# Performance work log

Measured on AMD Instinct MI355X. Metric: run time of the kernel, lower is better.

The kernel has to match this reference:

```python
import jax, jax.numpy as jnp
import numpy as np
from jax import lax

EPS = 1e-5
K = 32
S1, S2 = 512, 256


def bn_relu(x, gamma, beta, axes):
    # BatchNorm in training mode (batch statistics, biased variance) + ReLU.
    mean = jnp.mean(x, axis=axes, keepdims=True)
    var = jnp.var(x, axis=axes, keepdims=True)
    return jax.nn.relu((x - mean) * lax.rsqrt(var + EPS) * gamma + beta)


def fps(xyz, s):
    # Farthest point sampling, deterministic start at index 0. xyz: [N,3] -> [s] indices
    N = xyz.shape[0]
    def body(carry, _):
        dist, far = carry
        d = jnp.sum((xyz - xyz[far]) ** 2, axis=-1)
        dist = jnp.minimum(dist, d)
        return (dist, jnp.argmax(dist).astype(jnp.int32)), far
    init = (jnp.full((N,), 1e10, xyz.dtype), jnp.int32(0))
    _, idx = lax.scan(body, init, None, length=s)
    return idx


def sample_and_knn_group(s, k, coords, features):
    # coords: [B,N,3], features: [B,N,D]
    fps_idx = jax.vmap(lambda c: fps(c, s))(coords)                      # [B,s]
    new_xyz = jnp.take_along_axis(coords, fps_idx[..., None], axis=1)   # [B,s,3]
    new_feat = jnp.take_along_axis(features, fps_idx[..., None], axis=1)  # [B,s,D]
    # squared euclidean distances [B,s,N]
    d2 = (jnp.sum(new_xyz ** 2, -1)[..., None]
          - 2.0 * jnp.einsum('bsc,bnc->bsn', new_xyz, coords)
          + jnp.sum(coords ** 2, -1)[:, None, :])
    _, knn_idx = lax.top_k(-d2, k)                                       # [B,s,k]
    grouped = jax.vmap(lambda f, i: f[i])(features, knn_idx)             # [B,s,k,D]
    rel = grouped - new_feat[:, :, None, :]
    agg = jnp.concatenate([rel, jnp.broadcast_to(new_feat[:, :, None, :], rel.shape)], axis=-1)  # [B,s,k,2D]
    return new_xyz, agg


def sg_block(s, coords, feats, w1, cb1, g1, b1, w2, cb2, g2, b2):
    new_xyz, agg = sample_and_knn_group(s, K, coords, feats)
    h = bn_relu(jnp.einsum('bskc,oc->bsko', agg, w1) + cb1, g1, b1, (0, 1, 2))
    h = bn_relu(jnp.einsum('bskc,oc->bsko', h, w2) + cb2, g2, b2, (0, 1, 2))
    return new_xyz, jnp.max(h, axis=2)  # max over k neighbors -> [B,s,O]


def setup_inputs() -> dict:
    key = jax.random.key(0)
    ks = jax.random.split(key, 8)
    B, N = 16, 2048
    sc = 0.05
    return {
        'x': jax.random.normal(ks[0], (B, 3, N), jnp.float32),
        'emb_w1': jax.random.normal(ks[1], (64, 3), jnp.float32) * sc,
        'emb_g1': jnp.ones((64,), jnp.float32), 'emb_b1': jnp.zeros((64,), jnp.float32),
        'emb_w2': jax.random.normal(ks[2], (64, 64), jnp.float32) * sc,
        'emb_g2': jnp.ones((64,), jnp.float32), 'emb_b2': jnp.zeros((64,), jnp.float32),
        'sg1_w1': jax.random.normal(ks[3], (128, 128), jnp.float32) * sc,
        'sg1_cb1': jnp.zeros((128,), jnp.float32),
        'sg1_g1': jnp.ones((128,), jnp.float32), 'sg1_b1': jnp.zeros((128,), jnp.float32),
        'sg1_w2': jax.random.normal(ks[4], (128, 128), jnp.float32) * sc,
        'sg1_cb2': jnp.zeros((128,), jnp.float32),
        'sg1_g2': jnp.ones((128,), jnp.float32), 'sg1_b2': jnp.zeros((128,), jnp.float32),
        'sg2_w1': jax.random.normal(ks[5], (512, 256), jnp.float32) * sc,
        'sg2_cb1': jnp.zeros((512,), jnp.float32),
        'sg2_g1': jnp.ones((512,), jnp.float32), 'sg2_b1': jnp.zeros((512,), jnp.float32),
        'sg2_w2': jax.random.normal(ks[6], (512, 512), jnp.float32) * sc,
        'sg2_cb2': jnp.zeros((512,), jnp.float32),
        'sg2_g2': jnp.ones((512,), jnp.float32), 'sg2_b2': jnp.zeros((512,), jnp.float32),
    }


def reference(x, emb_w1, emb_g1, emb_b1, emb_w2, emb_g2, emb_b2,
              sg1_w1, sg1_cb1, sg1_g1, sg1_b1, sg1_w2, sg1_cb2, sg1_g2, sg1_b2,
              sg2_w1, sg2_cb1, sg2_g1, sg2_b1, sg2_w2, sg2_cb2, sg2_g2, sg2_b2):
    xyz = jnp.transpose(x, (0, 2, 1))  # [B,N,3]
    f = bn_relu(jnp.einsum('bnc,oc->bno', xyz, emb_w1), emb_g1, emb_b1, (0, 1))   # [B,N,64]
    f = bn_relu(jnp.einsum('bnc,oc->bno', f, emb_w2), emb_g2, emb_b2, (0, 1))
    xyz1, f1 = sg_block(S1, xyz, f, sg1_w1, sg1_cb1, sg1_g1, sg1_b1,
                        sg1_w2, sg1_cb2, sg1_g2, sg1_b2)   # [B,512,128]
    _, f2 = sg_block(S2, xyz1, f1, sg2_w1, sg2_cb1, sg2_g1, sg2_b1,
                     sg2_w2, sg2_cb2, sg2_g2, sg2_b2)      # [B,256,512]
    return jnp.transpose(f2, (0, 2, 1))  # [B,512,256] to match torch [B,C,s]
```

## Files before the change

### kernel.cpp

```cpp
#include <hip/hip_runtime.h>
#include <hip/hip_bf16.h>

#define EPS_BN 1e-5f
constexpr int BB = 16, NN = 2048, SS1 = 512, SS2 = 256, KNb = 32;

typedef short bf16x8 __attribute__((ext_vector_type(8)));
typedef float f32x4 __attribute__((ext_vector_type(4)));

__device__ inline float bflo(unsigned u) { return __uint_as_float(u << 16); }
__device__ inline float bfhi(unsigned u) { return __uint_as_float(u & 0xffff0000u); }
__device__ inline unsigned short f2bf_bits(float v) {
  __hip_bfloat16 h = __float2bfloat16(v);
  return *reinterpret_cast<unsigned short*>(&h);
}
__device__ inline unsigned fmono(float v) {
  int b = __float_as_int(v);
  return (unsigned)(b ^ ((b >> 31) | 0x80000000));
}

template <int CTRL>
__device__ inline void dpp_step_min(unsigned& hi, unsigned& lo) {
  unsigned hs = (unsigned)__builtin_amdgcn_update_dpp((int)hi, (int)hi, CTRL, 0xF, 0xF, false);
  unsigned ls = (unsigned)__builtin_amdgcn_update_dpp((int)lo, (int)lo, CTRL, 0xF, 0xF, false);
  bool take = (hs < hi) || (hs == hi && ls < lo);
  hi = take ? hs : hi; lo = take ? ls : lo;
}
template <int CTRL>
__device__ inline void dpp_step_maxv_minidx(unsigned& hi, unsigned& lo) {
  unsigned hs = (unsigned)__builtin_amdgcn_update_dpp((int)hi, (int)hi, CTRL, 0xF, 0xF, false);
  unsigned ls = (unsigned)__builtin_amdgcn_update_dpp((int)lo, (int)lo, CTRL, 0xF, 0xF, false);
  bool take = (hs > hi) || (hs == hi && ls < lo);
  hi = take ? hs : hi; lo = take ? ls : lo;
}
__device__ inline void dpp_chain_min(unsigned& hi, unsigned& lo) {
  dpp_step_min<0x111>(hi, lo); dpp_step_min<0x112>(hi, lo);
  dpp_step_min<0x114>(hi, lo); dpp_step_min<0x118>(hi, lo);
  dpp_step_min<0x142>(hi, lo); dpp_step_min<0x143>(hi, lo);
}
__device__ inline void dpp_chain_maxv_minidx(unsigned& hi, unsigned& lo) {
  dpp_step_maxv_minidx<0x111>(hi, lo); dpp_step_maxv_minidx<0x112>(hi, lo);
  dpp_step_maxv_minidx<0x114>(hi, lo); dpp_step_maxv_minidx<0x118>(hi, lo);
  dpp_step_maxv_minidx<0x142>(hi, lo); dpp_step_maxv_minidx<0x143>(hi, lo);
}
__device__ inline int dpp_reduce_min_idx(unsigned hi, unsigned lo) {
  dpp_chain_min(hi, lo);
  return __builtin_amdgcn_readlane((int)lo, 63);
}

__global__ void k_transpose(const float* __restrict__ x, float* __restrict__ xyz) {
  int idx = blockIdx.x * blockDim.x + threadIdx.x;
  if (idx >= BB * NN * 3) return;
  int c = idx % 3; int n = (idx / 3) % NN; int b = idx / (3 * NN);
  xyz[idx] = x[((size_t)b * 3 + c) * NN + n];
}

__global__ void k_emb1(const float* __restrict__ xyz, const float* __restrict__ w,
                       float* __restrict__ out) {
  int idx = blockIdx.x * blockDim.x + threadIdx.x;
  if (idx >= BB * NN * 64) return;
  int o = idx & 63; int pt = idx >> 6;
  const float* p = xyz + (size_t)pt * 3;
  const float* wr = w + o * 3;
  out[idx] = p[0] * wr[0] + p[1] * wr[1] + p[2] * wr[2];
}

__global__ void k_emb2(const float* __restrict__ fin, const float* __restrict__ w,
                       float* __restrict__ out) {
  int idx = blockIdx.x * blockDim.x + threadIdx.x;
  if (idx >= BB * NN * 64) return;
  int o = idx & 63; int pt = idx >> 6;
  const float* f = fin + (size_t)pt * 64;
  const float* wr = w + o * 64;
  float acc = 0.f;
#pragma unroll
  for (int c = 0; c < 64; c++) acc += f[c] * wr[c];
  out[idx] = acc;
}

__global__ __launch_bounds__(256) void k_stats_co(const float* __restrict__ d,
                                                  double* __restrict__ rsum,
                                                  double* __restrict__ rsq) {
  __shared__ float ls[64], lq[64];
  int t = threadIdx.x;
  if (t < 64) { ls[t] = 0.f; lq[t] = 0.f; }
  __syncthreads();
  size_t base = (size_t)blockIdx.x * 8192 + t * 4;
  float a0 = 0, a1 = 0, a2 = 0, a3 = 0, q0 = 0, q1 = 0, q2 = 0, q3 = 0;
  for (int it = 0; it < 8; it++) {
    float4 v = *(const float4*)(d + base + (size_t)it * 1024);
    a0 += v.x; q0 += v.x * v.x;
    a1 += v.y; q1 += v.y * v.y;
    a2 += v.z; q2 += v.z * v.z;
    a3 += v.w; q3 += v.w * v.w;
  }
  int c0 = (t * 4) & 63;
  atomicAdd(&ls[c0], a0); atomicAdd(&lq[c0], q0);
  atomicAdd(&ls[c0 + 1], a1); atomicAdd(&lq[c0 + 1], q1);
  atomicAdd(&ls[c0 + 2], a2); atomicAdd(&lq[c0 + 2], q2);
  atomicAdd(&ls[c0 + 3], a3); atomicAdd(&lq[c0 + 3], q3);
  __syncthreads();
  if (t < 64) {
    int rep = blockIdx.x & 63;
    atomicAdd(&rsum[(size_t)rep * 64 + t], (double)ls[t]);
    atomicAdd(&rsq[(size_t)rep * 64 + t], (double)lq[t]);
  }
}

__global__ void k_normrelu(float* __restrict__ data, const float* __restrict__ scale,
                           const float* __restrict__ shift, int total, int O) {
  int idx = blockIdx.x * blockDim.x + threadIdx.x;
  if (idx >= total) return;
  int o = idx % O;
  data[idx] = fmaxf(data[idx] * scale[o] + shift[o], 0.f);
}

template <int N>
__global__ __launch_bounds__(256, 1) void k_fps_mw(const float* __restrict__ xyz, int S,
                                                   int* __restrict__ fpsidx,
                                                   float* __restrict__ newxyz) {
  constexpr int PPL = N / 256;
  int b = blockIdx.x; int t = threadIdx.x;
  int w = t >> 6;
  __shared__ float sx[N], sy[N], sz[N];
  __shared__ unsigned combH[2][4], combL[2][4];
  float px[PPL], py[PPL], pz[PPL], ds[PPL];
#pragma unroll
  for (int r = 0; r < PPL; r++) {
    int i = r * 256 + t;
    size_t base = ((size_t)b * N + i) * 3;
    float xx = xyz[base], yy = xyz[base + 1], zz = xyz[base + 2];
    px[r] = xx; py[r] = yy; pz[r] = zz;
    float ox = xx, oy = yy, oz = zz;
    asm volatile("" : "+v"(ox), "+v"(oy), "+v"(oz));
    sx[i] = ox; sy[i] = oy; sz[i] = oz;
    ds[r] = 1e10f;
  }
  __syncthreads();
  int far = 0; int p = 0;
  for (int it = 0; it < S; it++) {
    float fx = sx[far], fy = sy[far], fz = sz[far];
    if (t == 0) {
      fpsidx[b * S + it] = far;
      size_t ob = ((size_t)b * S + it) * 3;
      newxyz[ob] = fx; newxyz[ob + 1] = fy; newxyz[ob + 2] = fz;
    }
    float mv0 = -1.f, mv1 = -1.f, mv2 = -1.f, mv3 = -1.f;
    int mi0 = 0, mi1 = 0, mi2 = 0, mi3 = 0;
#pragma unroll
    for (int r = 0; r < PPL; r++) {
      float dx = px[r] - fx, dy = py[r] - fy, dz = pz[r] - fz;
      float d = dx * dx + dy * dy + dz * dz;
      float nd = d < ds[r] ? d : ds[r];
      ds[r] = nd;
      int gi = r * 256 + t;
      if ((r & 3) == 0) { bool tk = nd > mv0; mv0 = tk ? nd : mv0; mi0 = tk ? gi : mi0; }
      else if ((r & 3) == 1) { bool tk = nd > mv1; mv1 = tk ? nd : mv1; mi1 = tk ? gi : mi1; }
      else if ((r & 3) == 2) { bool tk = nd > mv2; mv2 = tk ? nd : mv2; mi2 = tk ? gi : mi2; }
      else { bool tk = nd > mv3; mv3 = tk ? nd : mv3; mi3 = tk ? gi : mi3; }
    }
    { bool tk = (mv1 > mv0) || (mv1 == mv0 && mi1 < mi0);
      mv0 = tk ? mv1 : mv0; mi0 = tk ? mi1 : mi0; }
    { bool tk = (mv3 > mv2) || (mv3 == mv2 && mi3 < mi2);
      mv2 = tk ? mv3 : mv2; mi2 = tk ? mi3 : mi2; }
    { bool tk = (mv2 > mv0) || (mv2 == mv0 && mi2 < mi0);
      mv0 = tk ? mv2 : mv0; mi0 = tk ? mi2 : mi0; }
    unsigned hi = __float_as_uint(mv0);
    unsigned lo = (unsigned)mi0;
    dpp_chain_maxv_minidx(hi, lo);
    unsigned rh = (unsigned)__builtin_amdgcn_readlane((int)hi, 63);
    unsigned rl = (unsigned)__builtin_amdgcn_readlane((int)lo, 63);
    combH[p][w] = rh;
    combL[p][w] = rl;
    __syncthreads();
    unsigned bh = combH[p][0], bl = combL[p][0];
#pragma unroll
    for (int ww = 1; ww < 4; ww++) {
      unsigned oh = combH[p][ww], ol = combL[p][ww];
      bool take = (oh > bh) || (oh == bh && ol < bl);
      bh = take ? oh : bh; bl = take ? ol : bl;
    }
    far = (int)bl;
    p ^= 1;
  }
}

template <int N, int S>
__global__ __launch_bounds__(64, 1) void k_knn_wave(const float* __restrict__ pts,
                                                    const float* __restrict__ ctr,
                                                    int* __restrict__ knn) {
  constexpr int PPL = N / 64;
  int blk = blockIdx.x; int lane = threadIdx.x;
  int b = blk / S;
  float cx = ctr[(size_t)blk * 3], cy = ctr[(size_t)blk * 3 + 1], cz = ctr[(size_t)blk * 3 + 2];
  float cn = cx * cx + cy * cy + cz * cz;
  float d2[PPL];
#pragma unroll
  for (int r = 0; r < PPL; r++) {
    int i = r * 64 + lane;
    size_t pb = ((size_t)b * N + i) * 3;
    float xx = pts[pb], yy = pts[pb + 1], zz = pts[pb + 2];
    d2[r] = cn - 2.f * (cx * xx + cy * yy + cz * zz) + (xx * xx + yy * yy + zz * zz);
  }
  for (int kk = 0; kk < KNb; kk++) {
    float a0 = d2[0], a1 = d2[1], a2 = d2[2], a3 = d2[3];
#pragma unroll
    for (int r = 4; r < PPL; r += 4) {
      a0 = fminf(a0, d2[r]); a1 = fminf(a1, d2[r + 1]);
      a2 = fminf(a2, d2[r + 2]); a3 = fminf(a3, d2[r + 3]);
    }
    float m = fminf(fminf(a0, a1), fminf(a2, a3));
    int cand[PPL];
#pragma unroll
    for (int r = 0; r < PPL; r++) cand[r] = (d2[r] == m) ? (r * 64 + lane) : 0x7fffffff;
#pragma unroll
    for (int st = PPL / 2; st > 0; st >>= 1)
#pragma unroll
      for (int r = 0; r < st; r++) cand[r] = cand[r] < cand[r + st] ? cand[r] : cand[r + st];
    int widx = dpp_reduce_min_idx(fmono(m), (unsigned)cand[0]);
    if (lane == 0) knn[(size_t)blk * KNb + kk] = widx;
    int wr = widx >> 6, wl = widx & 63;
#pragma unroll
    for (int r = 0; r < PPL; r++) d2[r] = (r == wr && lane == wl) ? 3.4e38f : d2[r];
  }
}

__global__ void k_f2bf(const float* __restrict__ w, __hip_bfloat16* __restrict__ o, int n) {
  int i = blockIdx.x * blockDim.x + threadIdx.x;
  if (i < n) o[i] = __float2bfloat16(w[i]);
}

template <int D>
__global__ __launch_bounds__(256) void k_gather(const float* __restrict__ feat, int N,
                                                const int* __restrict__ fpsidx,
                                                const int* __restrict__ knn, int S,
                                                __hip_bfloat16* __restrict__ A) {
  int blk = blockIdx.x; int b = blk / S; int t = threadIdx.x;
  __shared__ float cf[D]; __shared__ int nbr[KNb];
  if (t < KNb) nbr[t] = knn[(size_t)blk * KNb + t];
  int center = fpsidx[blk];
  for (int c = t; c < D; c += 256) cf[c] = feat[((size_t)b * N + center) * D + c];
  __syncthreads();
  for (int i = t; i < KNb * D; i += 256) {
    int kk = i / D, c = i - kk * D;
    float v = feat[((size_t)b * N + nbr[kk]) * D + c];
    size_t row = (size_t)blk * KNb + kk;
    A[row * (2 * D) + c] = __float2bfloat16(v - cf[c]);
    A[row * (2 * D) + D + c] = __float2bfloat16(cf[c]);
  }
}

template <int K, int EPI>
__global__ __launch_bounds__(256) void k_mgemm(
    const __hip_bfloat16* __restrict__ A, const __hip_bfloat16* __restrict__ W,
    int N, int Mtiles, const float* __restrict__ bias,
    __hip_bfloat16* __restrict__ Hout,
    float* __restrict__ maxb, float* __restrict__ minb,
    double* __restrict__ rsum, double* __restrict__ rsq) {
  constexpr int SP = 40;
  int bm = blockIdx.x % Mtiles; int bn = blockIdx.x / Mtiles;
  int t = threadIdx.x; int w = t >> 6; int lane = t & 63;
  int wm = w & 1, wn = w >> 1; int quad = lane >> 4; int l15 = lane & 15;
  __shared__ short As[128 * SP];
  __shared__ short Ws[128 * SP];
  f32x4 acc[4][4];
  f32x4 zero = {0.f, 0.f, 0.f, 0.f};
#pragma unroll
  for (int i = 0; i < 4; i++)
#pragma unroll
    for (int j = 0; j < 4; j++) acc[i][j] = zero;

  int srow = t >> 2, sseg = t & 3;
  const short* Ag = (const short*)A;
  const short* Wg = (const short*)W;
  size_t arow0 = (size_t)bm * 128;
  size_t wrow0 = (size_t)bn * 128;

  for (int k0 = 0; k0 < K; k0 += 32) {
    __syncthreads();
    uint4 a0 = *(const uint4*)(Ag + (arow0 + srow) * K + k0 + sseg * 8);
    uint4 a1 = *(const uint4*)(Ag + (arow0 + srow + 64) * K + k0 + sseg * 8);
    uint4 b0 = *(const uint4*)(Wg + (wrow0 + srow) * K + k0 + sseg * 8);
    uint4 b1 = *(const uint4*)(Wg + (wrow0 + srow + 64) * K + k0 + sseg * 8);
    *(uint4*)(As + srow * SP + sseg * 8) = a0;
    *(uint4*)(As + (srow + 64) * SP + sseg * 8) = a1;
    *(uint4*)(Ws + srow * SP + sseg * 8) = b0;
    *(uint4*)(Ws + (srow + 64) * SP + sseg * 8) = b1;
    __syncthreads();
    bf16x8 af[4], bfr[4];
#pragma unroll
    for (int i = 0; i < 4; i++)
      af[i] = *(const bf16x8*)(As + (wm * 64 + i * 16 + l15) * SP + quad * 8);
#pragma unroll
    for (int j = 0; j < 4; j++)
      bfr[j] = *(const bf16x8*)(Ws + (wn * 64 + j * 16 + l15) * SP + quad * 8);
#pragma unroll
    for (int i = 0; i < 4; i++)
#pragma unroll
      for (int j = 0; j < 4; j++)
        acc[i][j] = __builtin_amdgcn_mfma_f32_16x16x32_bf16(af[i], bfr[j], acc[i][j], 0, 0, 0);
  }

  if constexpr (EPI == 0) {
    int rep = blockIdx.x & 63;
#pragma unroll
    for (int j = 0; j < 4; j++) {
      int col = bn * 128 + wn * 64 + j * 16 + l15;
      float bs = bias[col];
      float su = 0.f, sq = 0.f;
#pragma unroll
      for (int i = 0; i < 4; i++)
#pragma unroll
        for (int r = 0; r < 4; r++) {
          int row = bm * 128 + wm * 64 + i * 16 + quad * 4 + r;
          float v = acc[i][j][r] + bs;
          Hout[(size_t)row * N + col] = __float2bfloat16(v);
          su += v; sq += v * v;
        }
      atomicAdd(&rsum[(size_t)rep * N + col], (double)su);
      atomicAdd(&rsq[(size_t)rep * N + col], (double)sq);
    }
  } else {
    __shared__ float buf[128][33];
    for (int s = 0; s < 4; s++) {
      __syncthreads();
      if (wn == (s >> 1)) {
        int jb = 2 * (s & 1);
#pragma unroll
        for (int jj = 0; jj < 2; jj++) {
          int j = jb + jj;
          int lcol = jj * 16 + l15;
          float bs = bias[bn * 128 + s * 32 + lcol];
#pragma unroll
          for (int i = 0; i < 4; i++)
#pragma unroll
            for (int r = 0; r < 4; r++)
              buf[wm * 64 + i * 16 + quad * 4 + r][lcol] = acc[i][j][r] + bs;
        }
      }
      __syncthreads();
      if (t < 128) {
        int g = t >> 5, c = t & 31;
        float mx = -3.4e38f, mn = 3.4e38f, su = 0.f, sq = 0.f;
#pragma unroll
        for (int r = 0; r < 32; r++) {
          float v = buf[g * 32 + r][c];
          mx = fmaxf(mx, v); mn = fminf(mn, v);
          su += v; sq += v * v;
        }
        int col = bn * 128 + s * 32 + c;
        size_t gidx = (size_t)bm * 4 + g;
        maxb[gidx * N + col] = mx;
        minb[gidx * N + col] = mn;
        int rep = blockIdx.x & 63;
        atomicAdd(&rsum[(size_t)rep * N + col], (double)su);
        atomicAdd(&rsq[(size_t)rep * N + col], (double)sq);
      }
    }
  }
}

__global__ __launch_bounds__(256) void k_bnrelu(__hip_bfloat16* __restrict__ Hm, int O, int iters,
                                                const float* __restrict__ sc,
                                                const float* __restrict__ sh) {
  int t = threadIdx.x;
  size_t base = (size_t)blockIdx.x * 2048 * iters + t * 8;
  int c0 = (t * 8) & (O - 1);
  float s[8], h[8];
#pragma unroll
  for (int j = 0; j < 8; j++) { s[j] = sc[c0 + j]; h[j] = sh[c0 + j]; }
  unsigned* Hu = (unsigned*)Hm;
  for (int it = 0; it < iters; it++) {
    size_t e = (base + (size_t)it * 2048) / 2;
    uint4 raw = *(uint4*)(Hu + e);
    unsigned ws_[4] = {raw.x, raw.y, raw.z, raw.w};
    unsigned out[4];
#pragma unroll
    for (int k = 0; k < 4; k++) {
      float v0 = fmaxf(bflo(ws_[k]) * s[2 * k] + h[2 * k], 0.f);
      float v1 = fmaxf(bfhi(ws_[k]) * s[2 * k + 1] + h[2 * k + 1], 0.f);
      out[k] = (unsigned)f2bf_bits(v0) | ((unsigned)f2bf_bits(v1) << 16);
    }
    uint4 o4 = {out[0], out[1], out[2], out[3]};
    *(uint4*)(Hu + e) = o4;
  }
}

__global__ void k_finalize(const double* __restrict__ rsum, const double* __restrict__ rsq,
                           int O, int rows,
                           const float* __restrict__ gamma, const float* __restrict__ beta,
                           float* __restrict__ scale, float* __restrict__ shift) {
  int o = blockIdx.x * blockDim.x + threadIdx.x;
  if (o >= O) return;
  double s = 0, s2 = 0;
  for (int r = 0; r < 64; r++) { s += rsum[(size_t)r * O + o]; s2 += rsq[(size_t)r * O + o]; }
  double mean = s / rows;
  double var = s2 / rows - mean * mean;
  float sc = gamma[o] * rsqrtf((float)var + EPS_BN);
  scale[o] = sc; shift[o] = beta[o] - (float)mean * sc;
}

__global__ void k_final_feat(const float* __restrict__ maxb, const float* __restrict__ minb,
                             const float* __restrict__ scale, const float* __restrict__ shift,
                             float* __restrict__ out, int total, int O) {
  int idx = blockIdx.x * blockDim.x + threadIdx.x;
  if (idx >= total) return;
  int o = idx % O; float sc = scale[o];
  float sel = sc > 0.f ? maxb[idx] : minb[idx];
  out[idx] = fmaxf(sel * sc + shift[o], 0.f);
}

__global__ void k_final_out(const float* __restrict__ maxb, const float* __restrict__ minb,
                            const float* __restrict__ scale, const float* __restrict__ shift,
                            float* __restrict__ out) {
  int idx = blockIdx.x * blockDim.x + threadIdx.x;
  if (idx >= BB * SS2 * 512) return;
  int o = idx % 512; int si = (idx / 512) % SS2; int b = idx / (512 * SS2);
  float sc = scale[o];
  float sel = sc > 0.f ? maxb[idx] : minb[idx];
  out[((size_t)b * 512 + o) * SS2 + si] = fmaxf(sel * sc + shift[o], 0.f);
}

extern "C" void kernel_launch(void* const* d_in, const int* in_sizes, int n_in,
                              void* d_out, int out_size, void* d_ws, size_t ws_size,
                              hipStream_t stream) {
  const float* x       = (const float*)d_in[0];
  const float* emb_w1  = (const float*)d_in[1];
  const float* emb_g1  = (const float*)d_in[2];
  const float* emb_b1  = (const float*)d_in[3];
  const float* emb_w2  = (const float*)d_in[4];
  const float* emb_g2  = (const float*)d_in[5];
  const float* emb_b2  = (const float*)d_in[6];
  const float* sg1_w1  = (const float*)d_in[7];
  const float* sg1_cb1 = (const float*)d_in[8];
  const float* sg1_g1  = (const float*)d_in[9];
  const float* sg1_b1  = (const float*)d_in[10];
  const float* sg1_w2  = (const float*)d_in[11];
  const float* sg1_cb2 = (const float*)d_in[12];
  const float* sg1_g2  = (const float*)d_in[13];
  const float* sg1_b2  = (const float*)d_in[14];
  const float* sg2_w1  = (const float*)d_in[15];
  const float* sg2_cb1 = (const float*)d_in[16];
  const float* sg2_g1  = (const float*)d_in[17];
  const float* sg2_b1  = (const float*)d_in[18];
  const float* sg2_w2  = (const float*)d_in[19];
  const float* sg2_cb2 = (const float*)d_in[20];
  const float* sg2_g2  = (const float*)d_in[21];
  const float* sg2_b2  = (const float*)d_in[22];

  char* ws = (char*)d_ws;
  size_t off = 0;
  auto alloc = [&](size_t bytes) -> size_t {
    size_t cur = off; off += (bytes + 255) & ~(size_t)255; return cur;
  };
  float* xyz  = (float*)(ws + alloc((size_t)BB * NN * 3 * 4));
  float* fA   = (float*)(ws + alloc((size_t)BB * NN * 64 * 4));
  float* fB   = (float*)(ws + alloc((size_t)BB * NN * 64 * 4));
  float* f1   = (float*)(ws + alloc((size_t)BB * SS1 * 128 * 4));
  float* nx1  = (float*)(ws + alloc((size_t)BB * SS1 * 3 * 4));
  float* nx2  = (float*)(ws + alloc((size_t)BB * SS2 * 3 * 4));
  int* fps1   = (int*)(ws + alloc((size_t)BB * SS1 * 4));
  int* fps2   = (int*)(ws + alloc((size_t)BB * SS2 * 4));
  int* knn1   = (int*)(ws + alloc((size_t)BB * SS1 * KNb * 4));
  int* knn2   = (int*)(ws + alloc((size_t)BB * SS2 * KNb * 4));
  float* maxb = (float*)(ws + alloc((size_t)BB * SS2 * 512 * 4));
  float* minb = (float*)(ws + alloc((size_t)BB * SS2 * 512 * 4));
  float* scbuf = (float*)(ws + alloc((size_t)12 * 512 * 4));
  float* sc11 = scbuf + 4 * 512, *sh11 = scbuf + 5 * 512;
  float* sc12 = scbuf + 6 * 512, *sh12 = scbuf + 7 * 512;
  float* sc21 = scbuf + 8 * 512, *sh21 = scbuf + 9 * 512;
  float* sc22 = scbuf + 10 * 512, *sh22 = scbuf + 11 * 512;
  float* sc_e1 = scbuf + 0 * 512, *sh_e1 = scbuf + 1 * 512;
  float* sc_e2 = scbuf + 2 * 512, *sh_e2 = scbuf + 3 * 512;
  size_t statsz = (size_t)12 * 64 * 512 * 8;
  char* statz = ws + alloc(statsz);
  double* st = (double*)statz;
  double* rsA = st + 0 * 64 * 512, *rqA = st + 1 * 64 * 512;
  double* rsB = st + 2 * 64 * 512, *rqB = st + 3 * 64 * 512;
  double* rsC = st + 4 * 64 * 512, *rqC = st + 5 * 64 * 512;
  double* rsD = st + 6 * 64 * 512, *rqD = st + 7 * 64 * 512;
  double* rsE1 = st + 8 * 64 * 512, *rqE1 = st + 9 * 64 * 512;
  double* rsE2 = st + 10 * 64 * 512, *rqE2 = st + 11 * 64 * 512;
  __hip_bfloat16* wb11 = (__hip_bfloat16*)(ws + alloc(128 * 128 * 2));
  __hip_bfloat16* wb12 = (__hip_bfloat16*)(ws + alloc(128 * 128 * 2));
  __hip_bfloat16* wb21 = (__hip_bfloat16*)(ws + alloc(512 * 256 * 2));
  __hip_bfloat16* wb22 = (__hip_bfloat16*)(ws + alloc(512 * 512 * 2));
  __hip_bfloat16* Abuf = (__hip_bfloat16*)(ws + alloc((size_t)262144 * 128 * 2));
  __hip_bfloat16* Hbuf = (__hip_bfloat16*)(ws + alloc((size_t)131072 * 512 * 2));

  hipMemsetAsync(statz, 0, statsz, stream);

  const int thr = 256;
  k_transpose<<<(BB * NN * 3 + thr - 1) / thr, thr, 0, stream>>>(x, xyz);
  k_emb1<<<(BB * NN * 64 + thr - 1) / thr, thr, 0, stream>>>(xyz, emb_w1, fA);
  k_stats_co<<<256, 256, 0, stream>>>(fA, rsE1, rqE1);
  k_finalize<<<1, 64, 0, stream>>>(rsE1, rqE1, 64, BB * NN, emb_g1, emb_b1, sc_e1, sh_e1);
  k_normrelu<<<(BB * NN * 64 + thr - 1) / thr, thr, 0, stream>>>(fA, sc_e1, sh_e1, BB * NN * 64, 64);
  k_emb2<<<(BB * NN * 64 + thr - 1) / thr, thr, 0, stream>>>(fA, emb_w2, fB);
  k_stats_co<<<256, 256, 0, stream>>>(fB, rsE2, rqE2);
  k_finalize<<<1, 64, 0, stream>>>(rsE2, rqE2, 64, BB * NN, emb_g2, emb_b2, sc_e2, sh_e2);
  k_normrelu<<<(BB * NN * 64 + thr - 1) / thr, thr, 0, stream>>>(fB, sc_e2, sh_e2, BB * NN * 64, 64);

  k_f2bf<<<(128 * 128 + 255) / 256, 256, 0, stream>>>(sg1_w1, wb11, 128 * 128);
  k_f2bf<<<(128 * 128 + 255) / 256, 256, 0, stream>>>(sg1_w2, wb12, 128 * 128);
  k_f2bf<<<(512 * 256 + 255) / 256, 256, 0, stream>>>(sg2_w1, wb21, 512 * 256);
  k_f2bf<<<(512 * 512 + 255) / 256, 256, 0, stream>>>(sg2_w2, wb22, 512 * 512);

  k_fps_mw<NN><<<BB, 256, 0, stream>>>(xyz, SS1, fps1, nx1);
  k_knn_wave<NN, SS1><<<BB * SS1, 64, 0, stream>>>(xyz, nx1, knn1);

  k_gather<64><<<BB * SS1, 256, 0, stream>>>(fB, NN, fps1, knn1, SS1, Abuf);
  k_mgemm<128, 0><<<2048, 256, 0, stream>>>(Abuf, wb11, 128, 2048, sg1_cb1, Hbuf,
                                            nullptr, nullptr, rsA, rqA);
  k_finalize<<<1, 128, 0, stream>>>(rsA, rqA, 128, 262144, sg1_g1, sg1_b1, sc11, sh11);
  k_bnrelu<<<1024, 256, 0, stream>>>(Hbuf, 128, 16, sc11, sh11);
  k_mgemm<128, 1><<<2048, 256, 0, stream>>>(Hbuf, wb12, 128, 2048, sg1_cb2, nullptr,
                                            maxb, minb, rsB, rqB);
  k_finalize<<<1, 128, 0, stream>>>(rsB, rqB, 128, 262144, sg1_g2, sg1_b2, sc12, sh12);
  k_final_feat<<<(BB * SS1 * 128 + thr - 1) / thr, thr, 0, stream>>>(maxb, minb, sc12, sh12,
                                                                     f1, BB * SS1 * 128, 128);

  k_fps_mw<SS1><<<BB, 256, 0, stream>>>(nx1, SS2, fps2, nx2);
  k_knn_wave<SS1, SS2><<<BB * SS2, 64, 0, stream>>>(nx1, nx2, knn2);

  k_gather<128><<<BB * SS2, 256, 0, stream>>>(f1, SS1, fps2, knn2, SS2, Abuf);
  k_mgemm<256, 0><<<1024 * 4, 256, 0, stream>>>(Abuf, wb21, 512, 1024, sg2_cb1, Hbuf,
                                                nullptr, nullptr, rsC, rqC);
  k_finalize<<<4, 128, 0, stream>>>(rsC, rqC, 512, 131072, sg2_g1, sg2_b1, sc21, sh21);
  k_bnrelu<<<2048, 256, 0, stream>>>(Hbuf, 512, 16, sc21, sh21);
  k_mgemm<512, 1><<<1024 * 4, 256, 0, stream>>>(Hbuf, wb22, 512, 1024, sg2_cb2, nullptr,
                                                maxb, minb, rsD, rqD);
  k_finalize<<<4, 128, 0, stream>>>(rsD, rqD, 512, 131072, sg2_g2, sg2_b2, sc22, sh22);
  k_final_out<<<(BB * SS2 * 512 + thr - 1) / thr, thr, 0, stream>>>(maxb, minb, sc22, sh22,
                                                                    (float*)d_out);
}
```

Baseline: 1.465 ms.

## Fuse BN+ReLU into next GEMM's A-load and streamline FPS argmax

Removes the standalone k_bnrelu passes and instead applies the batch-norm scale/shift and ReLU to A tiles as they are loaded in the second GEMM of each block, using per-channel scale/shift staged in shared memory. This drops a full read-modify-write of the hidden activation buffer. The second GEMM redoes the normalization once per N-tile (several times for the 512-wide layer), which adds ALU work in the load path. FPS also packs xyz into a float4 in shared memory and splits the argmax into a max-value pass followed by a min-index tree, to cut per-point select work in the serial loop.

New measurement: 1.339 ms. 1.09x faster.

```diff
diff --git a/kernel.cpp b/kernel.cpp
--- a/kernel.cpp
+++ b/kernel.cpp
@@ -16,6 +16,11 @@
 __device__ inline unsigned fmono(float v) {
   int b = __float_as_int(v);
   return (unsigned)(b ^ ((b >> 31) | 0x80000000));
+}
+__device__ inline unsigned bn2(unsigned u, float s0, float h0, float s1, float h1) {
+  float v0 = fmaxf(bflo(u) * s0 + h0, 0.f);
+  float v1 = fmaxf(bfhi(u) * s1 + h1, 0.f);
+  return (unsigned)f2bf_bits(v0) | ((unsigned)f2bf_bits(v1) << 16);
 }
 
 template <int CTRL>
@@ -121,7 +126,7 @@
   constexpr int PPL = N / 256;
   int b = blockIdx.x; int t = threadIdx.x;
   int w = t >> 6;
-  __shared__ float sx[N], sy[N], sz[N];
+  __shared__ float4 sxyz[N];
   __shared__ unsigned combH[2][4], combL[2][4];
   float px[PPL], py[PPL], pz[PPL], ds[PPL];
 #pragma unroll
@@ -132,40 +137,42 @@
     px[r] = xx; py[r] = yy; pz[r] = zz;
     float ox = xx, oy = yy, oz = zz;
     asm volatile("" : "+v"(ox), "+v"(oy), "+v"(oz));
-    sx[i] = ox; sy[i] = oy; sz[i] = oz;
+    float4 o4 = {ox, oy, oz, 0.f};
+    sxyz[i] = o4;
     ds[r] = 1e10f;
   }
   __syncthreads();
   int far = 0; int p = 0;
   for (int it = 0; it < S; it++) {
-    float fx = sx[far], fy = sy[far], fz = sz[far];
+    float4 f4 = sxyz[far];
+    float fx = f4.x, fy = f4.y, fz = f4.z;
     if (t == 0) {
       fpsidx[b * S + it] = far;
       size_t ob = ((size_t)b * S + it) * 3;
       newxyz[ob] = fx; newxyz[ob + 1] = fy; newxyz[ob + 2] = fz;
     }
-    float mv0 = -1.f, mv1 = -1.f, mv2 = -1.f, mv3 = -1.f;
-    int mi0 = 0, mi1 = 0, mi2 = 0, mi3 = 0;
+    float mm0 = -1.f, mm1 = -1.f, mm2 = -1.f, mm3 = -1.f;
 #pragma unroll
     for (int r = 0; r < PPL; r++) {
       float dx = px[r] - fx, dy = py[r] - fy, dz = pz[r] - fz;
       float d = dx * dx + dy * dy + dz * dz;
       float nd = d < ds[r] ? d : ds[r];
       ds[r] = nd;
-      int gi = r * 256 + t;
-      if ((r & 3) == 0) { bool tk = nd > mv0; mv0 = tk ? nd : mv0; mi0 = tk ? gi : mi0; }
-      else if ((r & 3) == 1) { bool tk = nd > mv1; mv1 = tk ? nd : mv1; mi1 = tk ? gi : mi1; }
-      else if ((r & 3) == 2) { bool tk = nd > mv2; mv2 = tk ? nd : mv2; mi2 = tk ? gi : mi2; }
-      else { bool tk = nd > mv3; mv3 = tk ? nd : mv3; mi3 = tk ? gi : mi3; }
-    }
-    { bool tk = (mv1 > mv0) || (mv1 == mv0 && mi1 < mi0);
-      mv0 = tk ? mv1 : mv0; mi0 = tk ? mi1 : mi0; }
-    { bool tk = (mv3 > mv2) || (mv3 == mv2 && mi3 < mi2);
-      mv2 = tk ? mv3 : mv2; mi2 = tk ? mi3 : mi2; }
-    { bool tk = (mv2 > mv0) || (mv2 == mv0 && mi2 < mi0);
-      mv0 = tk ? mv2 : mv0; mi0 = tk ? mi2 : mi0; }
-    unsigned hi = __float_as_uint(mv0);
-    unsigned lo = (unsigned)mi0;
+      if ((r & 3) == 0) mm0 = nd > mm0 ? nd : mm0;
+      else if ((r & 3) == 1) mm1 = nd > mm1 ? nd : mm1;
+      else if ((r & 3) == 2) mm2 = nd > mm2 ? nd : mm2;
+      else mm3 = nd > mm3 ? nd : mm3;
+    }
+    float m = fmaxf(fmaxf(mm0, mm1), fmaxf(mm2, mm3));
+    int cand[PPL];
+#pragma unroll
+    for (int r = 0; r < PPL; r++) cand[r] = (ds[r] == m) ? (r * 256 + t) : 0x7fffffff;
+#pragma unroll
+    for (int st = PPL / 2; st > 0; st >>= 1)
+#pragma unroll
+      for (int r = 0; r < st; r++) cand[r] = cand[r] < cand[r + st] ? cand[r] : cand[r + st];
+    unsigned hi = __float_as_uint(m);
+    unsigned lo = (unsigned)cand[0];
     dpp_chain_maxv_minidx(hi, lo);
     unsigned rh = (unsigned)__builtin_amdgcn_readlane((int)hi, 63);
     unsigned rl = (unsigned)__builtin_amdgcn_readlane((int)lo, 63);
@@ -249,10 +256,11 @@
   }
 }
 
-template <int K, int EPI>
+template <int K, int EPI, bool BNA>
 __global__ __launch_bounds__(256) void k_mgemm(
     const __hip_bfloat16* __restrict__ A, const __hip_bfloat16* __restrict__ W,
     int N, int Mtiles, const float* __restrict__ bias,
+    const float* __restrict__ bnsc, const float* __restrict__ bnsh,
     __hip_bfloat16* __restrict__ Hout,
     float* __restrict__ maxb, float* __restrict__ minb,
     double* __restrict__ rsum, double* __restrict__ rsq) {
@@ -262,6 +270,10 @@
   int wm = w & 1, wn = w >> 1; int quad = lane >> 4; int l15 = lane & 15;
   __shared__ short As[128 * SP];
   __shared__ short Ws[128 * SP];
+  __shared__ float scs[BNA ? K : 1], shs[BNA ? K : 1];
+  if constexpr (BNA) {
+    for (int i = t; i < K; i += 256) { scs[i] = bnsc[i]; shs[i] = bnsh[i]; }
+  }
   f32x4 acc[4][4];
   f32x4 zero = {0.f, 0.f, 0.f, 0.f};
 #pragma unroll
@@ -281,6 +293,20 @@
     uint4 a1 = *(const uint4*)(Ag + (arow0 + srow + 64) * K + k0 + sseg * 8);
     uint4 b0 = *(const uint4*)(Wg + (wrow0 + srow) * K + k0 + sseg * 8);
     uint4 b1 = *(const uint4*)(Wg + (wrow0 + srow + 64) * K + k0 + sseg * 8);
+    if constexpr (BNA) {
+      int cb = k0 + sseg * 8;
+      float s[8], h[8];
+#pragma unroll
+      for (int q = 0; q < 8; q++) { s[q] = scs[cb + q]; h[q] = shs[cb + q]; }
+      a0.x = bn2(a0.x, s[0], h[0], s[1], h[1]);
+      a0.y = bn2(a0.y, s[2], h[2], s[3], h[3]);
+      a0.z = bn2(a0.z, s[4], h[4], s[5], h[5]);
+      a0.w = bn2(a0.w, s[6], h[6], s[7], h[7]);
+      a1.x = bn2(a1.x, s[0], h[0], s[1], h[1]);
+      a1.y = bn2(a1.y, s[2], h[2], s[3], h[3]);
+      a1.z = bn2(a1.z, s[4], h[4], s[5], h[5]);
+      a1.w = bn2(a1.w, s[6], h[6], s[7], h[7]);
+    }
     *(uint4*)(As + srow * SP + sseg * 8) = a0;
     *(uint4*)(As + (srow + 64) * SP + sseg * 8) = a1;
     *(uint4*)(Ws + srow * SP + sseg * 8) = b0;
@@ -356,32 +382,6 @@
         atomicAdd(&rsq[(size_t)rep * N + col], (double)sq);
       }
     }
-  }
-}
-
-__global__ __launch_bounds__(256) void k_bnrelu(__hip_bfloat16* __restrict__ Hm, int O, int iters,
-                                                const float* __restrict__ sc,
-                                                const float* __restrict__ sh) {
-  int t = threadIdx.x;
-  size_t base = (size_t)blockIdx.x * 2048 * iters + t * 8;
-  int c0 = (t * 8) & (O - 1);
-  float s[8], h[8];
-#pragma unroll
-  for (int j = 0; j < 8; j++) { s[j] = sc[c0 + j]; h[j] = sh[c0 + j]; }
-  unsigned* Hu = (unsigned*)Hm;
-  for (int it = 0; it < iters; it++) {
-    size_t e = (base + (size_t)it * 2048) / 2;
-    uint4 raw = *(uint4*)(Hu + e);
-    unsigned ws_[4] = {raw.x, raw.y, raw.z, raw.w};
-    unsigned out[4];
-#pragma unroll
-    for (int k = 0; k < 4; k++) {
-      float v0 = fmaxf(bflo(ws_[k]) * s[2 * k] + h[2 * k], 0.f);
-      float v1 = fmaxf(bfhi(ws_[k]) * s[2 * k + 1] + h[2 * k + 1], 0.f);
-      out[k] = (unsigned)f2bf_bits(v0) | ((unsigned)f2bf_bits(v1) << 16);
-    }
-    uint4 o4 = {out[0], out[1], out[2], out[3]};
-    *(uint4*)(Hu + e) = o4;
   }
 }
 
@@ -509,12 +509,13 @@
   k_knn_wave<NN, SS1><<<BB * SS1, 64, 0, stream>>>(xyz, nx1, knn1);
 
   k_gather<64><<<BB * SS1, 256, 0, stream>>>(fB, NN, fps1, knn1, SS1, Abuf);
-  k_mgemm<128, 0><<<2048, 256, 0, stream>>>(Abuf, wb11, 128, 2048, sg1_cb1, Hbuf,
-                                            nullptr, nullptr, rsA, rqA);
+  k_mgemm<128, 0, false><<<2048, 256, 0, stream>>>(Abuf, wb11, 128, 2048, sg1_cb1,
+                                                   nullptr, nullptr, Hbuf,
+                                                   nullptr, nullptr, rsA, rqA);
   k_finalize<<<1, 128, 0, stream>>>(rsA, rqA, 128, 262144, sg1_g1, sg1_b1, sc11, sh11);
-  k_bnrelu<<<1024, 256, 0, stream>>>(Hbuf, 128, 16, sc11, sh11);
-  k_mgemm<128, 1><<<2048, 256, 0, stream>>>(Hbuf, wb12, 128, 2048, sg1_cb2, nullptr,
-                                            maxb, minb, rsB, rqB);
+  k_mgemm<128, 1, true><<<2048, 256, 0, stream>>>(Hbuf, wb12, 128, 2048, sg1_cb2,
+                                                  sc11, sh11, nullptr,
+                                                  maxb, minb, rsB, rqB);
   k_finalize<<<1, 128, 0, stream>>>(rsB, rqB, 128, 262144, sg1_g2, sg1_b2, sc12, sh12);
   k_final_feat<<<(BB * SS1 * 128 + thr - 1) / thr, thr, 0, stream>>>(maxb, minb, sc12, sh12,
                                                                      f1, BB * SS1 * 128, 128);
@@ -523,12 +524,13 @@
   k_knn_wave<SS1, SS2><<<BB * SS2, 64, 0, stream>>>(nx1, nx2, knn2);
 
   k_gather<128><<<BB * SS2, 256, 0, stream>>>(f1, SS1, fps2, knn2, SS2, Abuf);
-  k_mgemm<256, 0><<<1024 * 4, 256, 0, stream>>>(Abuf, wb21, 512, 1024, sg2_cb1, Hbuf,
-                                                nullptr, nullptr, rsC, rqC);
+  k_mgemm<256, 0, false><<<1024 * 4, 256, 0, stream>>>(Abuf, wb21, 512, 1024, sg2_cb1,
+                                                       nullptr, nullptr, Hbuf,
+                                                       nullptr, nullptr, rsC, rqC);
   k_finalize<<<4, 128, 0, stream>>>(rsC, rqC, 512, 131072, sg2_g1, sg2_b1, sc21, sh21);
-  k_bnrelu<<<2048, 256, 0, stream>>>(Hbuf, 512, 16, sc21, sh21);
-  k_mgemm<512, 1><<<1024 * 4, 256, 0, stream>>>(Hbuf, wb22, 512, 1024, sg2_cb2, nullptr,
-                                                maxb, minb, rsD, rqD);
+  k_mgemm<512, 1, true><<<1024 * 4, 256, 0, stream>>>(Hbuf, wb22, 512, 1024, sg2_cb2,
+                                                      sc21, sh21, nullptr,
+                                                      maxb, minb, rsD, rqD);
   k_finalize<<<4, 128, 0, stream>>>(rsD, rqD, 512, 131072, sg2_g2, sg2_b2, sc22, sh22);
   k_final_out<<<(BB * SS2 * 512 + thr - 1) / thr, thr, 0, stream>>>(maxb, minb, sc22, sh22,
                                                                     (float*)d_out);
```
